# Optimization experiments

Measured on AMD Instinct MI355X. Metric: run time of the kernel, lower is better.

The kernel has to match this reference:

```python
import jax, jax.numpy as jnp
import numpy as np

B, L, K, S, D, H, C = 32, 256, 50, 16, 128, 4, 128
V, NN, NU, NS = 50000, 100000, 50000, 5000


def mha(q, k, v, in_w, in_b, out_w, out_b, n_heads):
    # PyTorch nn.MultiheadAttention (batch_first, eval mode) semantics.
    d = q.shape[-1]
    hd = d // n_heads
    wq, wk, wv = jnp.split(in_w, 3, axis=0)
    bq, bk, bv = jnp.split(in_b, 3)
    def heads(t):
        return t.reshape(t.shape[:-1] + (n_heads, hd))
    qh = heads(q @ wq.T + bq)
    kh = heads(k @ wk.T + bk)
    vh = heads(v @ wv.T + bv)
    scores = jnp.einsum('...qhd,...khd->...hqk', qh, kh) / jnp.sqrt(jnp.asarray(hd, q.dtype))
    attn = jax.nn.softmax(scores, axis=-1)
    o = jnp.einsum('...hqk,...khd->...qhd', attn, vh)
    o = o.reshape(o.shape[:-2] + (d,))
    return o @ out_w.T + out_b


def conv1d(x, w, b):
    # x: [B, D, L], w: [Cout, D, k]
    y = jax.lax.conv_general_dilated(x, w, (1,), 'VALID', dimension_numbers=('NCH', 'OIH', 'NCH'))
    return y + b[None, :, None]


def meta_path_module(paths, gru_wih, gru_whh, gru_bih, gru_bhh, in_w, in_b, out_w, out_b, ln_g, ln_b):
    # paths: [B, S, T, D] -> [B, D]
    b, s, t, d = paths.shape
    x = paths.reshape(b * s, t, d)
    def step(h, xt):
        gi = xt @ gru_wih.T + gru_bih
        gh = h @ gru_whh.T + gru_bhh
        ir, iz, inn = jnp.split(gi, 3, axis=-1)
        hr, hz, hn = jnp.split(gh, 3, axis=-1)
        r = jax.nn.sigmoid(ir + hr)
        z = jax.nn.sigmoid(iz + hz)
        n = jnp.tanh(inn + r * hn)
        return (1.0 - z) * n + z * h, None
    h0 = jnp.zeros((b * s, d), paths.dtype)
    h, _ = jax.lax.scan(step, h0, jnp.swapaxes(x, 0, 1))
    enc = h.reshape(b, s, d)
    attn = mha(enc, enc, enc, in_w, in_b, out_w, out_b, H)
    y = enc + attn
    mu = jnp.mean(y, -1, keepdims=True)
    var = jnp.var(y, -1, keepdims=True)
    y = (y - mu) / jnp.sqrt(var + 1e-5) * ln_g + ln_b
    return jnp.mean(y, axis=1)


def _forward(word_table, news_table, user_table, source_table,
             wa_in_w, wa_in_b, wa_out_w, wa_out_b,
             conv_w3, conv_b3, conv_w4, conv_b4, conv_w5, conv_b5, fc_w, fc_b,
             nsn_gru_wih, nsn_gru_whh, nsn_gru_bih, nsn_gru_bhh,
             nsn_in_w, nsn_in_b, nsn_out_w, nsn_out_b, nsn_ln_g, nsn_ln_b,
             nun_gru_wih, nun_gru_whh, nun_gru_bih, nun_gru_bhh,
             nun_in_w, nun_in_b, nun_out_w, nun_out_b, nun_ln_g, nun_ln_b,
             mp_w1, mp_b1, mp_w2, mp_b2, cls_w1, cls_b1, cls_w2, cls_b2,
             news_ids, news_word_indices, word_ctx_ids, nsn_src, nsn_end, nun_usr, nun_end):
    # --- fine-grained word embeds: per-token query attending over context news ---
    base = word_table[news_word_indices]              # [B, L, D]
    ctx = news_table[word_ctx_ids]                    # [B, L, K, D] (dominant gather)
    q = base[:, :, None, :]                           # [B, L, 1, D]
    fine = mha(q, ctx, ctx, wa_in_w, wa_in_b, wa_out_w, wa_out_b, H)[:, :, 0, :]
    pad = (news_word_indices == 0)[..., None]
    doc = jnp.where(pad, jnp.zeros((), base.dtype), fine)   # padding_idx=0 -> zeros
    # --- coarse CNN encoder ---
    x = jnp.swapaxes(doc, 1, 2)                       # [B, D, L]
    pooled = [jnp.max(jax.nn.relu(conv1d(x, w, b)), axis=2)
              for w, b in ((conv_w3, conv_b3), (conv_w4, conv_b4), (conv_w5, conv_b5))]
    semantic = jnp.concatenate(pooled, axis=1) @ fc_w.T + fc_b   # [B, D]
    # --- meta-path interaction ---
    start = jnp.broadcast_to(news_table[news_ids][:, None, :], (B, S, D))
    nsn_paths = jnp.stack([start, source_table[nsn_src], news_table[nsn_end]], axis=2)
    nun_paths = jnp.stack([start, user_table[nun_usr], news_table[nun_end]], axis=2)
    nsn_e = meta_path_module(nsn_paths, nsn_gru_wih, nsn_gru_whh, nsn_gru_bih, nsn_gru_bhh,
                             nsn_in_w, nsn_in_b, nsn_out_w, nsn_out_b, nsn_ln_g, nsn_ln_b)
    nun_e = meta_path_module(nun_paths, nun_gru_wih, nun_gru_whh, nun_gru_bih, nun_gru_bhh,
                             nun_in_w, nun_in_b, nun_out_w, nun_out_b, nun_ln_g, nun_ln_b)
    stack = jnp.stack([nsn_e, nun_e], axis=1)         # [B, 2, D]
    sc = jnp.tanh(stack @ mp_w1.T + mp_b1) @ mp_w2.T + mp_b2
    w = jax.nn.softmax(sc, axis=1)
    struct = jnp.sum(stack * w, axis=1)
    comb = jnp.concatenate([semantic, struct], axis=1)
    hcls = jax.nn.relu(comb @ cls_w1.T + cls_b1)
    return hcls @ cls_w2.T + cls_b2                   # [B, 2]


def setup_inputs() -> dict:
    key = jax.random.key(0)
    ks = iter(jax.random.split(key, 80))
    def p(shape):
        return (jax.random.normal(next(ks), shape, jnp.float32) * 0.02)
    inp = {}
    inp['news_ids'] = jax.random.randint(next(ks), (B,), 0, NN)
    inp['news_word_indices'] = jax.random.randint(next(ks), (B, L), 0, V)
    inp['word_ctx_ids'] = jax.random.randint(next(ks), (B, L, K), 0, NN)
    inp['nsn_src'] = jax.random.randint(next(ks), (B, S), 0, NS)
    inp['nsn_end'] = jax.random.randint(next(ks), (B, S), 0, NN)
    inp['nun_usr'] = jax.random.randint(next(ks), (B, S), 0, NU)
    inp['nun_end'] = jax.random.randint(next(ks), (B, S), 0, NN)
    inp['word_table'] = p((V, D)).at[0].set(0.0)
    inp['news_table'] = p((NN, D))
    inp['user_table'] = p((NU, D))
    inp['source_table'] = p((NS, D))
    inp['wa_in_w'] = p((3 * D, D)); inp['wa_in_b'] = p((3 * D,))
    inp['wa_out_w'] = p((D, D)); inp['wa_out_b'] = p((D,))
    for k in (3, 4, 5):
        inp[f'conv_w{k}'] = p((C, D, k)); inp[f'conv_b{k}'] = p((C,))
    inp['fc_w'] = p((D, 3 * C)); inp['fc_b'] = p((D,))
    for pre in ('nsn', 'nun'):
        inp[f'{pre}_gru_wih'] = p((3 * D, D)); inp[f'{pre}_gru_whh'] = p((3 * D, D))
        inp[f'{pre}_gru_bih'] = p((3 * D,)); inp[f'{pre}_gru_bhh'] = p((3 * D,))
        inp[f'{pre}_in_w'] = p((3 * D, D)); inp[f'{pre}_in_b'] = p((3 * D,))
        inp[f'{pre}_out_w'] = p((D, D)); inp[f'{pre}_out_b'] = p((D,))
        inp[f'{pre}_ln_g'] = jnp.ones((D,), jnp.float32); inp[f'{pre}_ln_b'] = jnp.zeros((D,), jnp.float32)
    inp['mp_w1'] = p((D // 2, D)); inp['mp_b1'] = p((D // 2,))
    inp['mp_w2'] = p((1, D // 2)); inp['mp_b2'] = p((1,))
    inp['cls_w1'] = p((D, 2 * D)); inp['cls_b1'] = p((D,))
    inp['cls_w2'] = p((2, D)); inp['cls_b2'] = p((2,))
    return inp


def reference(word_table, news_table, user_table, source_table,
              wa_in_w, wa_in_b, wa_out_w, wa_out_b,
              conv_w3, conv_b3, conv_w4, conv_b4, conv_w5, conv_b5, fc_w, fc_b,
              nsn_gru_wih, nsn_gru_whh, nsn_gru_bih, nsn_gru_bhh,
              nsn_in_w, nsn_in_b, nsn_out_w, nsn_out_b, nsn_ln_g, nsn_ln_b,
              nun_gru_wih, nun_gru_whh, nun_gru_bih, nun_gru_bhh,
              nun_in_w, nun_in_b, nun_out_w, nun_out_b, nun_ln_g, nun_ln_b,
              mp_w1, mp_b1, mp_w2, mp_b2, cls_w1, cls_b1, cls_w2, cls_b2,
              news_ids, news_word_indices, word_ctx_ids, nsn_src, nsn_end, nun_usr, nun_end):
    return _forward(word_table, news_table, user_table, source_table,
                    wa_in_w, wa_in_b, wa_out_w, wa_out_b,
                    conv_w3, conv_b3, conv_w4, conv_b4, conv_w5, conv_b5, fc_w, fc_b,
                    nsn_gru_wih, nsn_gru_whh, nsn_gru_bih, nsn_gru_bhh,
                    nsn_in_w, nsn_in_b, nsn_out_w, nsn_out_b, nsn_ln_g, nsn_ln_b,
                    nun_gru_wih, nun_gru_whh, nun_gru_bih, nun_gru_bhh,
                    nun_in_w, nun_in_b, nun_out_w, nun_out_b, nun_ln_g, nun_ln_b,
                    mp_w1, mp_b1, mp_w2, mp_b2, cls_w1, cls_b1, cls_w2, cls_b2,
                    news_ids, news_word_indices, word_ctx_ids, nsn_src, nsn_end, nun_usr, nun_end)
```

## Files before the change

### kernel.cpp

```cpp
#include <hip/hip_runtime.h>
#include <hip/hip_bf16.h>

#define BB 32
#define LL 256
#define KC 50
#define SS 16
#define DD 128
#define NH 4
#define CC 128
#define VV 50000
#define NNN 100000
#define NUU 50000
#define NSS 5000

typedef __attribute__((ext_vector_type(8))) short bf16x8;
typedef __attribute__((ext_vector_type(8))) unsigned short u16x8;
typedef __attribute__((ext_vector_type(4))) float f32x4;

#define APAD 132

__device__ __forceinline__ float dot4(float4 a, float4 b){
  return a.x*b.x + a.y*b.y + a.z*b.z + a.w*b.w;
}

__device__ __forceinline__ unsigned short f2bf(float f){
  union { float f; unsigned int u; } v; v.f = f;
  unsigned int r = (v.u + 0x7FFFu + ((v.u >> 16) & 1u)) >> 16;
  return (unsigned short)r;
}
__device__ __forceinline__ float bf2f(unsigned short s){
  union { unsigned int u; float f; } v; v.u = ((unsigned int)s) << 16;
  return v.f;
}

__global__ __launch_bounds__(256) void k_prep(
    const float* __restrict__ w3, const float* __restrict__ w4,
    const float* __restrict__ w5,
    const float* __restrict__ wih0, const float* __restrict__ whh0,
    const float* __restrict__ wih1, const float* __restrict__ whh1,
    const float* __restrict__ in_w, const float* __restrict__ out_w,
    const float* __restrict__ inw0, const float* __restrict__ outw0,
    const float* __restrict__ inw1, const float* __restrict__ outw1,
    unsigned short* __restrict__ wb3, unsigned short* __restrict__ wb4,
    unsigned short* __restrict__ wb5, unsigned short* __restrict__ wgb,
    unsigned short* __restrict__ wab, unsigned short* __restrict__ wmh){
  int e = blockIdx.x*256 + threadIdx.x;
  if (e < CC*DD*3){ int c=e/(DD*3), rm=e%(DD*3), d=rm/3, jj=rm%3;
    wb3[((size_t)jj*CC + c)*DD + d] = f2bf(w3[e]); }
  if (e < CC*DD*4){ int c=e/(DD*4), rm=e%(DD*4), d=rm/4, jj=rm%4;
    wb4[((size_t)jj*CC + c)*DD + d] = f2bf(w4[e]); }
  if (e < CC*DD*5){ int c=e/(DD*5), rm=e%(DD*5), d=rm/5, jj=rm%5;
    wb5[((size_t)jj*CC + c)*DD + d] = f2bf(w5[e]); }
  if (e < 384*DD){
    wgb[e]          = f2bf(wih0[e]);
    wgb[49152 + e]  = f2bf(whh0[e]);
    wgb[98304 + e]  = f2bf(wih1[e]);
    wgb[147456 + e] = f2bf(whh1[e]);
    wab[e]          = f2bf(in_w[e]);
  }
  if (e >= 384*DD && e < 512*DD) wab[e] = f2bf(out_w[e - 384*DD]);
  if (e < 512*DD){
    float s0 = (e < 384*DD) ? inw0[e] : outw0[e - 384*DD];
    float s1 = (e < 384*DD) ? inw1[e] : outw1[e - 384*DD];
    wmh[e]                 = f2bf(s0);
    wmh[(size_t)512*DD + e] = f2bf(s1);
  }
}

__global__ __launch_bounds__(256) void k_projkv(
    const float* __restrict__ news, const unsigned short* __restrict__ wkvb,
    const float* __restrict__ in_b, unsigned short* __restrict__ nK,
    unsigned short* __restrict__ nV){
  const int tid  = threadIdx.x;
  const int wave = tid >> 6;
  const int lane = tid & 63;
  const int l15  = lane & 15;
  const int quad = lane >> 4;
  const int r0   = blockIdx.x * 16;
  const int nw0  = wave * 64;

  const float* src = news + (size_t)(r0 + l15)*DD + quad*8;
  bf16x8 afr[4];
  #pragma unroll
  for (int ks=0; ks<4; ks++){
    float4 v0 = *(const float4*)(src + ks*32);
    float4 v1 = *(const float4*)(src + ks*32 + 4);
    bf16x8 a;
    a[0]=(short)f2bf(v0.x); a[1]=(short)f2bf(v0.y); a[2]=(short)f2bf(v0.z); a[3]=(short)f2bf(v0.w);
    a[4]=(short)f2bf(v1.x); a[5]=(short)f2bf(v1.y); a[6]=(short)f2bf(v1.z); a[7]=(short)f2bf(v1.w);
    afr[ks] = a;
  }
  unsigned short* outp = (nw0 < 128) ? nK : nV;
  const int cbase = nw0 & 127;
  #pragma unroll
  for (int nt=0; nt<4; nt++){
    const int n0 = nw0 + nt*16;
    bf16x8 bfr[4];
    #pragma unroll
    for (int ks=0; ks<4; ks++)
      bfr[ks] = *(const bf16x8*)(wkvb + (size_t)(n0 + l15)*DD + ks*32 + quad*8);
    const float bias = in_b[128 + n0 + l15];
    f32x4 acc = {0.f,0.f,0.f,0.f};
    #pragma unroll
    for (int ks=0; ks<4; ks++)
      acc = __builtin_amdgcn_mfma_f32_16x16x32_bf16(afr[ks], bfr[ks], acc, 0,0,0);
    const int c = cbase + nt*16 + l15;
    #pragma unroll
    for (int r=0;r<4;r++)
      outp[(size_t)(r0 + quad*4 + r)*DD + c] = f2bf(acc[r] + bias);
  }
}

__global__ __launch_bounds__(64) void k_qh(
    const float* __restrict__ word_table, const int* __restrict__ widx,
    const unsigned short* __restrict__ wqb, const float* __restrict__ in_b,
    float* __restrict__ qh){
  const int lane = threadIdx.x;
  const int l15 = lane & 15, quad = lane >> 4;
  const int p0 = blockIdx.x * 16;
  const int row = widx[p0 + l15];
  const float* src = word_table + (size_t)row*DD + quad*8;
  bf16x8 afr[4];
  #pragma unroll
  for (int ks=0; ks<4; ks++){
    float4 v0 = *(const float4*)(src + ks*32);
    float4 v1 = *(const float4*)(src + ks*32 + 4);
    bf16x8 a;
    a[0]=(short)f2bf(v0.x); a[1]=(short)f2bf(v0.y); a[2]=(short)f2bf(v0.z); a[3]=(short)f2bf(v0.w);
    a[4]=(short)f2bf(v1.x); a[5]=(short)f2bf(v1.y); a[6]=(short)f2bf(v1.z); a[7]=(short)f2bf(v1.w);
    afr[ks] = a;
  }
  #pragma unroll
  for (int nt=0; nt<8; nt++){
    const int n0 = nt*16;
    bf16x8 bfr[4];
    #pragma unroll
    for (int ks=0; ks<4; ks++)
      bfr[ks] = *(const bf16x8*)(wqb + (size_t)(n0+l15)*DD + ks*32 + quad*8);
    const float bias = in_b[n0 + l15];
    f32x4 acc = {0.f,0.f,0.f,0.f};
    #pragma unroll
    for (int ks=0; ks<4; ks++)
      acc = __builtin_amdgcn_mfma_f32_16x16x32_bf16(afr[ks], bfr[ks], acc, 0,0,0);
    #pragma unroll
    for (int r=0;r<4;r++){
      int m = quad*4 + r;
      qh[(size_t)(p0+m)*DD + n0 + l15] = acc[r] + bias;
    }
  }
}

__global__ __launch_bounds__(64) void k_attn(
    const float* __restrict__ qh, const unsigned short* __restrict__ nK,
    const unsigned short* __restrict__ nV, const int* __restrict__ ctx_ids,
    unsigned short* __restrict__ o_out){
  const int p = blockIdx.x;
  const int lane = threadIdx.x;
  const int r = lane >> 4;
  const int g = lane & 15;
  const int h = g >> 2;
  __shared__ int ids[52];
  __shared__ float sc[NH][52];
  if (lane < KC) ids[lane] = ctx_ids[(size_t)p*KC + lane];
  float qv[8];
  {
    const float4* qp = (const float4*)(qh + (size_t)p*DD + g*8);
    float4 q0 = qp[0], q1 = qp[1];
    qv[0]=q0.x; qv[1]=q0.y; qv[2]=q0.z; qv[3]=q0.w;
    qv[4]=q1.x; qv[5]=q1.y; qv[6]=q1.z; qv[7]=q1.w;
  }
  __syncthreads();
  for (int kb=0; kb<13; kb++){
    int k2 = kb*4 + r;
    int row = ids[(k2 < KC) ? k2 : 0];
    u16x8 kv = *(const u16x8*)(nK + (size_t)row*DD + g*8);
    float pr = 0.f;
    #pragma unroll
    for (int j=0;j<8;j++) pr += qv[j]*bf2f(kv[j]);
    pr += __shfl_xor(pr, 1, 64);
    pr += __shfl_xor(pr, 2, 64);
    if ((g & 3) == 0 && k2 < KC) sc[h][k2] = pr;
  }
  __syncthreads();
  {
    const int hh = lane >> 4, kc = lane & 15;
    const float scale = 0.17677669529663687f;
    float mx = -1e30f;
    #pragma unroll
    for (int q4=0;q4<4;q4++){ int k2=kc+q4*16; if (k2<KC) mx = fmaxf(mx, sc[hh][k2]); }
    mx = fmaxf(mx, __shfl_xor(mx, 1, 64));
    mx = fmaxf(mx, __shfl_xor(mx, 2, 64));
    mx = fmaxf(mx, __shfl_xor(mx, 4, 64));
    mx = fmaxf(mx, __shfl_xor(mx, 8, 64));
    float sm = 0.f;
    float ev[4];
    #pragma unroll
    for (int q4=0;q4<4;q4++){
      int k2=kc+q4*16;
      ev[q4] = (k2<KC) ? __expf((sc[hh][k2]-mx)*scale) : 0.f;
      sm += ev[q4];
    }
    sm += __shfl_xor(sm, 1, 64);
    sm += __shfl_xor(sm, 2, 64);
    sm += __shfl_xor(sm, 4, 64);
    sm += __shfl_xor(sm, 8, 64);
    float inv = 1.f/sm;
    #pragma unroll
    for (int q4=0;q4<4;q4++){ int k2=kc+q4*16; if (k2<KC) sc[hh][k2] = ev[q4]*inv; }
  }
  __syncthreads();
  float acc[8];
  #pragma unroll
  for (int j=0;j<8;j++) acc[j]=0.f;
  for (int kb=0; kb<13; kb++){
    int k2 = kb*4 + r;
    int row = ids[(k2 < KC) ? k2 : 0];
    float w = (k2 < KC) ? sc[h][k2] : 0.f;
    u16x8 vv = *(const u16x8*)(nV + (size_t)row*DD + g*8);
    #pragma unroll
    for (int j=0;j<8;j++) acc[j] += w*bf2f(vv[j]);
  }
  #pragma unroll
  for (int j=0;j<8;j++){
    acc[j] += __shfl_xor(acc[j], 16, 64);
    acc[j] += __shfl_xor(acc[j], 32, 64);
  }
  if (r == 0){
    u16x8 o;
    #pragma unroll
    for (int j=0;j<8;j++) o[j] = f2bf(acc[j]);
    *(u16x8*)(o_out + (size_t)p*DD + g*8) = o;
  }
}

__global__ __launch_bounds__(64) void k_wo(
    const unsigned short* __restrict__ o_attn, const int* __restrict__ widx,
    const unsigned short* __restrict__ wob, const float* __restrict__ out_b,
    unsigned short* __restrict__ doc){
  const int lane = threadIdx.x;
  const int l15 = lane & 15, quad = lane >> 4;
  const int p0 = blockIdx.x * 16;
  bf16x8 afr[4];
  #pragma unroll
  for (int ks=0; ks<4; ks++)
    afr[ks] = *(const bf16x8*)(o_attn + (size_t)(p0+l15)*DD + ks*32 + quad*8);
  int msk[4];
  #pragma unroll
  for (int r=0;r<4;r++) msk[r] = widx[p0 + quad*4 + r];
  #pragma unroll
  for (int nt=0; nt<8; nt++){
    const int n0 = nt*16;
    bf16x8 bfr[4];
    #pragma unroll
    for (int ks=0; ks<4; ks++)
      bfr[ks] = *(const bf16x8*)(wob + (size_t)(n0+l15)*DD + ks*32 + quad*8);
    const float bias = out_b[n0 + l15];
    f32x4 acc = {0.f,0.f,0.f,0.f};
    #pragma unroll
    for (int ks=0; ks<4; ks++)
      acc = __builtin_amdgcn_mfma_f32_16x16x32_bf16(afr[ks], bfr[ks], acc, 0,0,0);
    #pragma unroll
    for (int r=0;r<4;r++){
      int m = quad*4 + r;
      doc[(size_t)(p0+m)*DD + n0 + l15] = (msk[r] == 0) ? (unsigned short)0
                                                        : f2bf(acc[r] + bias);
    }
  }
}

#define CROWS 68
#define CPAD 136
__global__ __launch_bounds__(256) void k_conv(
    const unsigned short* __restrict__ doc, const unsigned short* __restrict__ wb3,
    const unsigned short* __restrict__ wb4, const unsigned short* __restrict__ wb5,
    float* __restrict__ convp){
  __shared__ __align__(16) char smem[CROWS*CPAD*2];
  unsigned short* ds = (unsigned short*)smem;
  float* smf = (float*)smem;
  const int blk = blockIdx.x;
  const int chunk = blk & 3;
  const int j = (blk >> 2) % 3;
  const int b = blk / 12;
  const int kk = 3 + j;
  const int T = LL - kk + 1;
  const int t0 = chunk * 64;
  const int nrows = 64 + kk - 1;
  const unsigned short* wb = (j==0) ? wb3 : (j==1) ? wb4 : wb5;
  const int tid = threadIdx.x;
  for (int i = tid; i < nrows*16; i += 256){
    int row = i >> 4, q8 = i & 15;
    int gt = t0 + row;
    u16x8 v = (u16x8){0,0,0,0,0,0,0,0};
    if (gt < LL) v = *(const u16x8*)(doc + ((size_t)b*LL + gt)*DD + q8*8);
    *(u16x8*)(ds + row*CPAD + q8*8) = v;
  }
  __syncthreads();
  const int wave = tid >> 6;
  const int lane = tid & 63;
  const int l15  = lane & 15;
  const int quad = lane >> 4;
  f32x4 acc[8];
  #pragma unroll
  for (int nt=0;nt<8;nt++) acc[nt] = (f32x4){0.f,0.f,0.f,0.f};
  for (int jj=0; jj<kk; jj++){
    #pragma unroll
    for (int ks=0; ks<4; ks++){
      bf16x8 af = *(const bf16x8*)(ds + (wave*16 + l15 + jj)*CPAD + ks*32 + quad*8);
      #pragma unroll
      for (int nt=0; nt<8; nt++){
        bf16x8 bf = *(const bf16x8*)(wb + ((size_t)jj*CC + nt*16 + l15)*DD + ks*32 + quad*8);
        acc[nt] = __builtin_amdgcn_mfma_f32_16x16x32_bf16(af, bf, acc[nt], 0,0,0);
      }
    }
  }
  __syncthreads();
  #pragma unroll
  for (int nt=0; nt<8; nt++){
    float mx = -1e30f;
    #pragma unroll
    for (int r=0;r<4;r++){
      int t = t0 + wave*16 + quad*4 + r;
      mx = fmaxf(mx, (t < T) ? acc[nt][r] : -1e30f);
    }
    mx = fmaxf(mx, __shfl_xor(mx, 16, 64));
    mx = fmaxf(mx, __shfl_xor(mx, 32, 64));
    if (quad == 0) smf[wave*128 + nt*16 + l15] = mx;
  }
  __syncthreads();
  if (tid < 128){
    float m4 = fmaxf(fmaxf(smf[tid], smf[128+tid]), fmaxf(smf[256+tid], smf[384+tid]));
    convp[(((size_t)b*3 + j)*4 + chunk)*CC + tid] = m4;
  }
}

#define GSTR 392
__global__ __launch_bounds__(256) void k_gru(
    const float* __restrict__ news_table, const float* __restrict__ user_table,
    const float* __restrict__ source_table,
    const int* __restrict__ news_ids, const int* __restrict__ nsn_src,
    const int* __restrict__ nsn_end, const int* __restrict__ nun_usr,
    const int* __restrict__ nun_end,
    const unsigned short* __restrict__ wgb,
    const float* __restrict__ bih0, const float* __restrict__ bhh0,
    const float* __restrict__ bih1, const float* __restrict__ bhh1,
    float* __restrict__ enc){
  __shared__ __align__(16) unsigned short xs[16][CPAD];
  __shared__ __align__(16) unsigned short hs[16][CPAD];
  __shared__ float hf[8][128];
  __shared__ float gi[8][GSTR];
  __shared__ float gh[8][GSTR];
  const int blk = blockIdx.x;
  const int m  = blk >> 6;
  const int b  = (blk >> 1) & 31;
  const int s0 = (blk & 1) * 8;
  const int tid = threadIdx.x;
  const int wave = tid >> 6, lane = tid & 63, l15 = lane & 15, quad = lane >> 4;
  const unsigned short* Wih = wgb + (size_t)m*2*384*DD;
  const unsigned short* Whh = Wih + 384*DD;
  const float* bih = m ? bih1 : bih0;
  const float* bhh = m ? bhh1 : bhh0;
  for (int i=tid;i<16*CPAD;i+=256){ (&xs[0][0])[i]=0; (&hs[0][0])[i]=0; }
  for (int i=tid;i<8*128;i+=256) (&hf[0][0])[i]=0.f;
  __syncthreads();
  for (int t=0;t<3;t++){
    {
      int s = tid >> 5, j = tid & 31;
      int row; const float* tab;
      if (t==0){ row = news_ids[b]; tab = news_table; }
      else if (t==1){ row = m ? nun_usr[b*SS+s0+s] : nsn_src[b*SS+s0+s];
                      tab = m ? user_table : source_table; }
      else { row = m ? nun_end[b*SS+s0+s] : nsn_end[b*SS+s0+s]; tab = news_table; }
      float4 v = ((const float4*)(tab + (size_t)row*DD))[j];
      unsigned short* dp = &xs[s][j*4];
      dp[0]=f2bf(v.x); dp[1]=f2bf(v.y); dp[2]=f2bf(v.z); dp[3]=f2bf(v.w);
    }
    __syncthreads();
    bf16x8 ax[4], ah[4];
    #pragma unroll
    for (int ks=0;ks<4;ks++){
      ax[ks] = *(const bf16x8*)&xs[l15][ks*32+quad*8];
      ah[ks] = *(const bf16x8*)&hs[l15][ks*32+quad*8];
    }
    #pragma unroll
    for (int nt=0;nt<6;nt++){
      const int n0 = wave*96 + nt*16;
      f32x4 ga = {0.f,0.f,0.f,0.f}, ha = {0.f,0.f,0.f,0.f};
      #pragma unroll
      for (int ks=0;ks<4;ks++){
        bf16x8 bi = *(const bf16x8*)(Wih + (size_t)(n0+l15)*DD + ks*32+quad*8);
        ga = __builtin_amdgcn_mfma_f32_16x16x32_bf16(ax[ks], bi, ga, 0,0,0);
        bf16x8 bh = *(const bf16x8*)(Whh + (size_t)(n0+l15)*DD + ks*32+quad*8);
        ha = __builtin_amdgcn_mfma_f32_16x16x32_bf16(ah[ks], bh, ha, 0,0,0);
      }
      if (quad < 2){
        #pragma unroll
        for (int r=0;r<4;r++){
          gi[quad*4+r][n0+l15] = ga[r];
          gh[quad*4+r][n0+l15] = ha[r];
        }
      }
    }
    __syncthreads();
    #pragma unroll
    for (int k=0;k<4;k++){
      int it = tid + k*256;
      int s = it >> 7, g = it & 127;
      float rr = 1.f/(1.f+__expf(-(gi[s][g] + gh[s][g] + bih[g] + bhh[g])));
      float zz = 1.f/(1.f+__expf(-(gi[s][128+g] + gh[s][128+g] + bih[128+g] + bhh[128+g])));
      float nn = tanhf(gi[s][256+g] + bih[256+g] + rr*(gh[s][256+g] + bhh[256+g]));
      float hnew = (1.f-zz)*nn + zz*hf[s][g];
      hf[s][g] = hnew;
      hs[s][g] = f2bf(hnew);
    }
    __syncthreads();
  }
  {
    int s = tid >> 5, j = tid & 31;
    float4 v = ((const float4*)hf[s])[j];
    ((float4*)(enc + (((size_t)m*BB + b)*SS + (s0+s))*DD))[j] = v;
  }
}

#define MPAD 136
__global__ __launch_bounds__(256) void k_metamha(
    const float* __restrict__ enc,
    const unsigned short* __restrict__ wmh,
    const float* __restrict__ inb0, const float* __restrict__ outb0,
    const float* __restrict__ lng0, const float* __restrict__ lnb0,
    const float* __restrict__ inb1, const float* __restrict__ outb1,
    const float* __restrict__ lng1, const float* __restrict__ lnb1,
    float* __restrict__ meta_e){
  const int m = blockIdx.x >> 5;
  const int b = blockIdx.x & 31;
  const int tid = threadIdx.x;
  const int wave = tid >> 6, lane = tid & 63, l15 = lane & 15, quad = lane >> 4;
  const unsigned short* W = wmh + (size_t)m*512*DD;
  const float* in_b  = m ? inb1 : inb0;
  const float* out_b = m ? outb1 : outb0;
  const float* lng   = m ? lng1 : lng0;
  const float* lnb   = m ? lnb1 : lnb0;

  __shared__ __align__(16) unsigned short ebf[16][MPAD];
  __shared__ __align__(16) unsigned short qb[16][MPAD];
  __shared__ __align__(16) unsigned short kb[16][MPAD];
  __shared__ __align__(16) unsigned short ob[16][MPAD];
  __shared__ float vf[16][128];
  __shared__ float er[16][132];
  __shared__ float at[NH][16][16];
  __shared__ float mu[16], rs[16];
  __shared__ float part[2][128];

  const float* esrc = enc + ((size_t)m*BB + b)*SS*DD;
  for (int i = tid; i < 16*32; i += 256){
    int s = i >> 5, j = i & 31;
    float4 v = ((const float4*)esrc)[i];
    ((float4*)er[s])[j] = v;
    unsigned short* dp = &ebf[s][j*4];
    dp[0]=f2bf(v.x); dp[1]=f2bf(v.y); dp[2]=f2bf(v.z); dp[3]=f2bf(v.w);
  }
  __syncthreads();
  {
    bf16x8 ax[4];
    #pragma unroll
    for (int ks=0;ks<4;ks++) ax[ks] = *(const bf16x8*)&ebf[l15][ks*32+quad*8];
    #pragma unroll
    for (int nt=0; nt<6; nt++){
      const int n0 = wave*96 + nt*16;
      f32x4 acc = {0.f,0.f,0.f,0.f};
      #pragma unroll
      for (int ks=0;ks<4;ks++){
        bf16x8 bw = *(const bf16x8*)(W + (size_t)(n0+l15)*DD + ks*32+quad*8);
        acc = __builtin_amdgcn_mfma_f32_16x16x32_bf16(ax[ks], bw, acc, 0,0,0);
      }
      const float bias = in_b[n0+l15];
      const int col = n0 + l15;
      #pragma unroll
      for (int r=0;r<4;r++){
        int row = quad*4+r;
        float val = acc[r] + bias;
        if (n0 < 128)      qb[row][col]       = f2bf(val);
        else if (n0 < 256) kb[row][col-128]   = f2bf(val);
        else               vf[row][col-256]   = val;
      }
    }
  }
  __syncthreads();
  {
    const int h = wave;
    bf16x8 aq = *(const bf16x8*)&qb[l15][h*32 + quad*8];
    bf16x8 ak = *(const bf16x8*)&kb[l15][h*32 + quad*8];
    f32x4 z = {0.f,0.f,0.f,0.f};
    f32x4 acc = __builtin_amdgcn_mfma_f32_16x16x32_bf16(aq, ak, z, 0,0,0);
    #pragma unroll
    for (int r=0;r<4;r++)
      at[h][quad*4+r][l15] = acc[r] * 0.17677669529663687f;
  }
  __syncthreads();
  if (tid < 64){
    int h = tid>>4, qi = tid&15;
    float mx=-1e30f;
    #pragma unroll
    for (int ki=0;ki<16;ki++) mx = fmaxf(mx, at[h][qi][ki]);
    float sm=0.f;
    float ee[16];
    #pragma unroll
    for (int ki=0;ki<16;ki++){ ee[ki]=__expf(at[h][qi][ki]-mx); sm+=ee[ki]; }
    float inv=1.f/sm;
    #pragma unroll
    for (int ki=0;ki<16;ki++) at[h][qi][ki]=ee[ki]*inv;
  }
  __syncthreads();
  {
    int c = tid & 127, h = c >> 5;
    int sBase = (tid >> 7) * 8;
    #pragma unroll
    for (int s=0;s<8;s++){
      float acc=0.f;
      #pragma unroll
      for (int ki=0;ki<16;ki++) acc += at[h][sBase+s][ki]*vf[ki][c];
      ob[sBase+s][c] = f2bf(acc);
    }
  }
  __syncthreads();
  {
    bf16x8 ao[4];
    #pragma unroll
    for (int ks=0;ks<4;ks++) ao[ks] = *(const bf16x8*)&ob[l15][ks*32+quad*8];
    #pragma unroll
    for (int nt=0; nt<2; nt++){
      const int n0 = wave*32 + nt*16;
      f32x4 acc = {0.f,0.f,0.f,0.f};
      #pragma unroll
      for (int ks=0;ks<4;ks++){
        bf16x8 bw = *(const bf16x8*)(W + (size_t)(384 + n0+l15)*DD + ks*32+quad*8);
        acc = __builtin_amdgcn_mfma_f32_16x16x32_bf16(ao[ks], bw, acc, 0,0,0);
      }
      const float bias = out_b[n0+l15];
      const int col = n0 + l15;
      #pragma unroll
      for (int r=0;r<4;r++){
        int row = quad*4 + r;
        er[row][col] += acc[r] + bias;
      }
    }
  }
  __syncthreads();
  {
    int row = tid >> 4, i = tid & 15;
    const float* yr = &er[row][i*8];
    float s1=0.f, s2=0.f;
    #pragma unroll
    for (int j2=0;j2<8;j2++){ float y=yr[j2]; s1+=y; s2+=y*y; }
    #pragma unroll
    for (int msk=1; msk<16; msk<<=1){
      s1 += __shfl_xor(s1, msk, 64);
      s2 += __shfl_xor(s2, msk, 64);
    }
    if (i==0){
      float mean = s1*(1.f/128.f);
      mu[row]=mean;
      rs[row]=rsqrtf(s2*(1.f/128.f) - mean*mean + 1e-5f);
    }
  }
  __syncthreads();
  {
    int c = tid & 127, half = tid >> 7;
    float g = lng[c], bb2 = lnb[c];
    float acc=0.f;
    #pragma unroll
    for (int s=0;s<8;s++){
      int ss = half*8+s;
      acc += (er[ss][c]-mu[ss])*rs[ss]*g + bb2;
    }
    part[half][c]=acc;
  }
  __syncthreads();
  if (tid < 128)
    meta_e[((size_t)m*BB+b)*DD + tid] = (part[0][tid]+part[1][tid]) * (1.f/16.f);
}

__global__ __launch_bounds__(128) void k_final(
    const float* __restrict__ convp,
    const float* __restrict__ cb3, const float* __restrict__ cb4,
    const float* __restrict__ cb5,
    const float* __restrict__ fc_w, const float* __restrict__ fc_b,
    const float* __restrict__ meta_e,
    const float* __restrict__ mp_w1, const float* __restrict__ mp_b1,
    const float* __restrict__ mp_w2, const float* __restrict__ mp_b2,
    const float* __restrict__ cls_w1, const float* __restrict__ cls_b1,
    const float* __restrict__ cls_w2, const float* __restrict__ cls_b2,
    float* __restrict__ out){
  const int b = blockIdx.x;
  const int c = threadIdx.x;
  __shared__ float pooled[384];
  __shared__ float comb[256];
  __shared__ float hcls[128];
  __shared__ float tt[2][64];
  __shared__ float wsc[2];
  for (int idx=c; idx<384; idx+=128){
    int j = idx >> 7, cc2 = idx & 127;
    const float* base = convp + (((size_t)b*3 + j)*4)*CC + cc2;
    float mx = -1e30f;
    for (int ci=0;ci<4;ci++) mx = fmaxf(mx, base[ci*CC]);
    const float* cb = (j==0)?cb3:(j==1)?cb4:cb5;
    pooled[idx] = fmaxf(mx + cb[cc2], 0.f);
  }
  __syncthreads();
  {
    float acc = fc_b[c];
    const float* wr = fc_w + (size_t)c*384;
    for (int i=0;i<384;i++) acc += pooled[i]*wr[i];
    comb[c] = acc;
  }
  if (c < 64){
    for (int m=0;m<2;m++){
      const float* ev = meta_e + ((size_t)m*BB+b)*DD;
      float acc = mp_b1[c];
      const float* wr = mp_w1 + (size_t)c*DD;
      for (int i=0;i<DD;i++) acc += ev[i]*wr[i];
      tt[m][c] = tanhf(acc);
    }
  }
  __syncthreads();
  if (c == 0){
    float s0 = mp_b2[0], s1 = mp_b2[0];
    for (int j=0;j<64;j++){ s0 += tt[0][j]*mp_w2[j]; s1 += tt[1][j]*mp_w2[j]; }
    float mx = fmaxf(s0,s1);
    float e0 = __expf(s0-mx), e1 = __expf(s1-mx);
    wsc[0] = e0/(e0+e1); wsc[1] = e1/(e0+e1);
  }
  __syncthreads();
  comb[128+c] = wsc[0]*meta_e[((size_t)b)*DD + c]
              + wsc[1]*meta_e[((size_t)(BB+b))*DD + c];
  __syncthreads();
  {
    float acc = cls_b1[c];
    const float* wr = cls_w1 + (size_t)c*256;
    for (int i=0;i<256;i++) acc += comb[i]*wr[i];
    hcls[c] = fmaxf(acc, 0.f);
  }
  __syncthreads();
  if (c < 2){
    float acc = cls_b2[c];
    const float* wr = cls_w2 + (size_t)c*DD;
    for (int i=0;i<DD;i++) acc += hcls[i]*wr[i];
    out[b*2 + c] = acc;
  }
}

extern "C" void kernel_launch(void* const* d_in, const int* in_sizes, int n_in,
                              void* d_out, int out_size, void* d_ws, size_t ws_size,
                              hipStream_t stream){
  const int* news_ids = (const int*)d_in[0];
  const int* nwi      = (const int*)d_in[1];
  const int* ctx_ids  = (const int*)d_in[2];
  const int* nsn_src  = (const int*)d_in[3];
  const int* nsn_end  = (const int*)d_in[4];
  const int* nun_usr  = (const int*)d_in[5];
  const int* nun_end  = (const int*)d_in[6];
  const float* word_table   = (const float*)d_in[7];
  const float* news_table   = (const float*)d_in[8];
  const float* user_table   = (const float*)d_in[9];
  const float* source_table = (const float*)d_in[10];
  const float* wa_in_w  = (const float*)d_in[11];
  const float* wa_in_b  = (const float*)d_in[12];
  const float* wa_out_w = (const float*)d_in[13];
  const float* wa_out_b = (const float*)d_in[14];
  const float* conv_w3 = (const float*)d_in[15];
  const float* conv_b3 = (const float*)d_in[16];
  const float* conv_w4 = (const float*)d_in[17];
  const float* conv_b4 = (const float*)d_in[18];
  const float* conv_w5 = (const float*)d_in[19];
  const float* conv_b5 = (const float*)d_in[20];
  const float* fc_w = (const float*)d_in[21];
  const float* fc_b = (const float*)d_in[22];
  const float* wih0 = (const float*)d_in[23];
  const float* whh0 = (const float*)d_in[24];
  const float* bih0 = (const float*)d_in[25];
  const float* bhh0 = (const float*)d_in[26];
  const float* inw0 = (const float*)d_in[27];
  const float* inb0 = (const float*)d_in[28];
  const float* outw0 = (const float*)d_in[29];
  const float* outb0 = (const float*)d_in[30];
  const float* lng0 = (const float*)d_in[31];
  const float* lnb0 = (const float*)d_in[32];
  const float* wih1 = (const float*)d_in[33];
  const float* whh1 = (const float*)d_in[34];
  const float* bih1 = (const float*)d_in[35];
  const float* bhh1 = (const float*)d_in[36];
  const float* inw1 = (const float*)d_in[37];
  const float* inb1 = (const float*)d_in[38];
  const float* outw1 = (const float*)d_in[39];
  const float* outb1 = (const float*)d_in[40];
  const float* lng1 = (const float*)d_in[41];
  const float* lnb1 = (const float*)d_in[42];
  const float* mp_w1 = (const float*)d_in[43];
  const float* mp_b1 = (const float*)d_in[44];
  const float* mp_w2 = (const float*)d_in[45];
  const float* mp_b2 = (const float*)d_in[46];
  const float* cls_w1 = (const float*)d_in[47];
  const float* cls_b1 = (const float*)d_in[48];
  const float* cls_w2 = (const float*)d_in[49];
  const float* cls_b2 = (const float*)d_in[50];

  char* wsb = (char*)d_ws;
  unsigned short* nK = (unsigned short*)wsb;
  unsigned short* nV = nK + (size_t)NNN*DD;
  unsigned short* wb3 = nV + (size_t)NNN*DD;
  unsigned short* wb4 = wb3 + (size_t)CC*DD*3;
  unsigned short* wb5 = wb4 + (size_t)CC*DD*4;
  unsigned short* wgb = wb5 + (size_t)CC*DD*5;
  unsigned short* wab = wgb + (size_t)4*384*DD;
  unsigned short* wmh = wab + (size_t)512*DD;
  float* qh     = (float*)(wmh + (size_t)2*512*DD);
  unsigned short* o_at = (unsigned short*)(qh + (size_t)BB*LL*DD);
  unsigned short* doc  = (unsigned short*)((float*)o_at + (size_t)BB*LL*DD);
  float* convp  = (float*)doc + (size_t)BB*LL*DD;
  float* enc    = convp + BB*3*4*CC;
  float* meta_e = enc + (size_t)2*BB*SS*DD;
  const size_t need_bytes = (size_t)((char*)(meta_e + 2*BB*DD) - wsb);
  if (ws_size < need_bytes) return;

  const unsigned short* wqb  = wab;
  const unsigned short* wkvb = wab + (size_t)128*DD;
  const unsigned short* wob  = wab + (size_t)384*DD;

  k_prep<<<dim3(320), dim3(256), 0, stream>>>(conv_w3, conv_w4, conv_w5,
      wih0, whh0, wih1, whh1, wa_in_w, wa_out_w,
      inw0, outw0, inw1, outw1,
      wb3, wb4, wb5, wgb, wab, wmh);
  k_projkv<<<dim3(NNN/16), dim3(256), 0, stream>>>(news_table, wkvb, wa_in_b, nK, nV);
  k_qh<<<dim3(BB*LL/16), dim3(64), 0, stream>>>(word_table, nwi, wqb, wa_in_b, qh);
  k_attn<<<dim3(BB*LL), dim3(64), 0, stream>>>(qh, nK, nV, ctx_ids, o_at);
  k_wo<<<dim3(BB*LL/16), dim3(64), 0, stream>>>(o_at, nwi, wob, wa_out_b, doc);
  k_conv<<<dim3(BB*3*4), dim3(256), 0, stream>>>(doc, wb3, wb4, wb5, convp);
  k_gru<<<dim3(128), dim3(256), 0, stream>>>(news_table, user_table, source_table,
      news_ids, nsn_src, nsn_end, nun_usr, nun_end,
      wgb, bih0, bhh0, bih1, bhh1, enc);
  k_metamha<<<dim3(64), dim3(256), 0, stream>>>(enc, wmh,
      inb0, outb0, lng0, lnb0,
      inb1, outb1, lng1, lnb1, meta_e);
  k_final<<<dim3(BB), dim3(128), 0, stream>>>(convp, conv_b3, conv_b4, conv_b5,
      fc_w, fc_b, meta_e, mp_w1, mp_b1, mp_w2, mp_b2,
      cls_w1, cls_b1, cls_w2, cls_b2, (float*)d_out);
}
```

Baseline: 404.7 us.

## Restructure K/V projection to one wave per tile with LDS-staged coalesced stores

The K/V projection kernel now runs one wave per 16-row tile instead of four waves that each reload the same activation rows. The MFMA operands are swapped so each lane holds four consecutive output columns, which allows vectorized bias loads and packed 8-byte writes into shared memory. Output rows are then written to global memory as coalesced 8-byte stores instead of scattered 2-byte stores. In exchange, each wave does four times more MFMA work serially, and the kernel gains a shared-memory round trip and a barrier.

```diff
diff --git a/kernel.cpp b/kernel.cpp
--- a/kernel.cpp
+++ b/kernel.cpp
@@ -67,18 +67,15 @@
   }
 }
 
-__global__ __launch_bounds__(256) void k_projkv(
+#define PKSTR 272
+__global__ __launch_bounds__(64) void k_projkv(
     const float* __restrict__ news, const unsigned short* __restrict__ wkvb,
     const float* __restrict__ in_b, unsigned short* __restrict__ nK,
     unsigned short* __restrict__ nV){
-  const int tid  = threadIdx.x;
-  const int wave = tid >> 6;
-  const int lane = tid & 63;
-  const int l15  = lane & 15;
-  const int quad = lane >> 4;
-  const int r0   = blockIdx.x * 16;
-  const int nw0  = wave * 64;
-
+  __shared__ __align__(16) unsigned short os[16*PKSTR];
+  const int lane = threadIdx.x;
+  const int l15 = lane & 15, quad = lane >> 4;
+  const int r0 = blockIdx.x * 16;
   const float* src = news + (size_t)(r0 + l15)*DD + quad*8;
   bf16x8 afr[4];
   #pragma unroll
@@ -90,24 +87,32 @@
     a[4]=(short)f2bf(v1.x); a[5]=(short)f2bf(v1.y); a[6]=(short)f2bf(v1.z); a[7]=(short)f2bf(v1.w);
     afr[ks] = a;
   }
-  unsigned short* outp = (nw0 < 128) ? nK : nV;
-  const int cbase = nw0 & 127;
-  #pragma unroll
-  for (int nt=0; nt<4; nt++){
-    const int n0 = nw0 + nt*16;
-    bf16x8 bfr[4];
+  #pragma unroll
+  for (int nt=0; nt<16; nt++){
+    const int n0 = nt*16;
+    bf16x8 wfr[4];
     #pragma unroll
     for (int ks=0; ks<4; ks++)
-      bfr[ks] = *(const bf16x8*)(wkvb + (size_t)(n0 + l15)*DD + ks*32 + quad*8);
-    const float bias = in_b[128 + n0 + l15];
+      wfr[ks] = *(const bf16x8*)(wkvb + (size_t)(n0 + l15)*DD + ks*32 + quad*8);
     f32x4 acc = {0.f,0.f,0.f,0.f};
     #pragma unroll
     for (int ks=0; ks<4; ks++)
-      acc = __builtin_amdgcn_mfma_f32_16x16x32_bf16(afr[ks], bfr[ks], acc, 0,0,0);
-    const int c = cbase + nt*16 + l15;
-    #pragma unroll
-    for (int r=0;r<4;r++)
-      outp[(size_t)(r0 + quad*4 + r)*DD + c] = f2bf(acc[r] + bias);
+      acc = __builtin_amdgcn_mfma_f32_16x16x32_bf16(wfr[ks], afr[ks], acc, 0,0,0);
+    float4 bias = *(const float4*)(in_b + 128 + n0 + quad*4);
+    unsigned short pk[4];
+    pk[0] = f2bf(acc[0] + bias.x);
+    pk[1] = f2bf(acc[1] + bias.y);
+    pk[2] = f2bf(acc[2] + bias.z);
+    pk[3] = f2bf(acc[3] + bias.w);
+    *(unsigned long long*)(os + l15*PKSTR + n0 + quad*4) = *(const unsigned long long*)pk;
+  }
+  __syncthreads();
+  unsigned short* outp = (lane < 32) ? nK : nV;
+  const int col = (lane*4) & 127;
+  #pragma unroll
+  for (int j=0; j<16; j++){
+    unsigned long long v = *(const unsigned long long*)(os + j*PKSTR + lane*4);
+    *(unsigned long long*)(outp + (size_t)(r0 + j)*DD + col) = v;
   }
 }
 
@@ -729,7 +734,7 @@
       wih0, whh0, wih1, whh1, wa_in_w, wa_out_w,
       inw0, outw0, inw1, outw1,
       wb3, wb4, wb5, wgb, wab, wmh);
-  k_projkv<<<dim3(NNN/16), dim3(256), 0, stream>>>(news_table, wkvb, wa_in_b, nK, nV);
+  k_projkv<<<dim3(NNN/16), dim3(64), 0, stream>>>(news_table, wkvb, wa_in_b, nK, nV);
   k_qh<<<dim3(BB*LL/16), dim3(64), 0, stream>>>(word_table, nwi, wqb, wa_in_b, qh);
   k_attn<<<dim3(BB*LL), dim3(64), 0, stream>>>(qh, nK, nV, ctx_ids, o_at);
   k_wo<<<dim3(BB*LL/16), dim3(64), 0, stream>>>(o_at, nwi, wob, wa_out_b, doc);
```

Result: faster. 390.4 us (-3.5%).

## Tile K/V projection over 80 rows per block with register-resident weights and staged stores

Applied to the files above, without the earlier changes.

The K/V projection kernel now processes 80 news rows per block instead of 16. Each wave keeps its 64x128 weight slice in registers for five row tiles, and the fp32 inputs are converted to bf16 once into shared memory. The MFMA operands are swapped so results come out transposed, then staged through LDS so each lane writes 8-byte contiguous chunks to global memory. This amortizes weight loads and improves store coalescing, at the cost of more registers and LDS per block and fewer blocks in the grid.

```diff
diff --git a/kernel.cpp b/kernel.cpp
--- a/kernel.cpp
+++ b/kernel.cpp
@@ -67,47 +67,76 @@
   }
 }
 
+#define PST 136
+#define TST 72
 __global__ __launch_bounds__(256) void k_projkv(
     const float* __restrict__ news, const unsigned short* __restrict__ wkvb,
     const float* __restrict__ in_b, unsigned short* __restrict__ nK,
     unsigned short* __restrict__ nV){
+  __shared__ __align__(16) unsigned short As[80*PST];
+  __shared__ __align__(16) unsigned short Tw[4*16*TST];
   const int tid  = threadIdx.x;
   const int wave = tid >> 6;
   const int lane = tid & 63;
   const int l15  = lane & 15;
   const int quad = lane >> 4;
-  const int r0   = blockIdx.x * 16;
-  const int nw0  = wave * 64;
-
-  const float* src = news + (size_t)(r0 + l15)*DD + quad*8;
-  bf16x8 afr[4];
-  #pragma unroll
-  for (int ks=0; ks<4; ks++){
-    float4 v0 = *(const float4*)(src + ks*32);
-    float4 v1 = *(const float4*)(src + ks*32 + 4);
-    bf16x8 a;
-    a[0]=(short)f2bf(v0.x); a[1]=(short)f2bf(v0.y); a[2]=(short)f2bf(v0.z); a[3]=(short)f2bf(v0.w);
-    a[4]=(short)f2bf(v1.x); a[5]=(short)f2bf(v1.y); a[6]=(short)f2bf(v1.z); a[7]=(short)f2bf(v1.w);
-    afr[ks] = a;
-  }
-  unsigned short* outp = (nw0 < 128) ? nK : nV;
-  const int cbase = nw0 & 127;
-  #pragma unroll
-  for (int nt=0; nt<4; nt++){
-    const int n0 = nw0 + nt*16;
-    bf16x8 bfr[4];
+  const int r0   = blockIdx.x * 80;
+  const int cw   = wave * 64;
+
+  bf16x8 wfr[4][4];
+  #pragma unroll
+  for (int nt=0; nt<4; nt++)
     #pragma unroll
     for (int ks=0; ks<4; ks++)
-      bfr[ks] = *(const bf16x8*)(wkvb + (size_t)(n0 + l15)*DD + ks*32 + quad*8);
-    const float bias = in_b[128 + n0 + l15];
-    f32x4 acc = {0.f,0.f,0.f,0.f};
+      wfr[nt][ks] = *(const bf16x8*)(wkvb + (size_t)(cw + nt*16 + l15)*DD + ks*32 + quad*8);
+  float4 bv[4];
+  #pragma unroll
+  for (int nt=0; nt<4; nt++)
+    bv[nt] = *(const float4*)(in_b + 128 + cw + nt*16 + quad*4);
+
+  for (int i = tid; i < 80*32; i += 256){
+    int row = i >> 5, j = i & 31;
+    float4 v = ((const float4*)(news + (size_t)(r0 + row)*DD))[j];
+    unsigned short* d = As + row*PST + j*4;
+    d[0]=f2bf(v.x); d[1]=f2bf(v.y); d[2]=f2bf(v.z); d[3]=f2bf(v.w);
+  }
+  __syncthreads();
+
+  unsigned short* outp = (wave < 2) ? nK : nV;
+  const int cwo = (wave & 1) * 64;
+  unsigned short* tw = Tw + wave*16*TST;
+  const int rr = lane >> 4;
+  const int cc = lane & 15;
+
+  #pragma unroll
+  for (int mt=0; mt<5; mt++){
+    bf16x8 afr[4];
     #pragma unroll
     for (int ks=0; ks<4; ks++)
-      acc = __builtin_amdgcn_mfma_f32_16x16x32_bf16(afr[ks], bfr[ks], acc, 0,0,0);
-    const int c = cbase + nt*16 + l15;
-    #pragma unroll
-    for (int r=0;r<4;r++)
-      outp[(size_t)(r0 + quad*4 + r)*DD + c] = f2bf(acc[r] + bias);
+      afr[ks] = *(const bf16x8*)(As + (mt*16 + l15)*PST + ks*32 + quad*8);
+    f32x4 acc[4];
+    #pragma unroll
+    for (int nt=0; nt<4; nt++) acc[nt] = (f32x4){0.f,0.f,0.f,0.f};
+    #pragma unroll
+    for (int ks=0; ks<4; ks++)
+      #pragma unroll
+      for (int nt=0; nt<4; nt++)
+        acc[nt] = __builtin_amdgcn_mfma_f32_16x16x32_bf16(wfr[nt][ks], afr[ks], acc[nt], 0,0,0);
+    #pragma unroll
+    for (int nt=0; nt<4; nt++){
+      unsigned short pk[4];
+      pk[0] = f2bf(acc[nt][0] + bv[nt].x);
+      pk[1] = f2bf(acc[nt][1] + bv[nt].y);
+      pk[2] = f2bf(acc[nt][2] + bv[nt].z);
+      pk[3] = f2bf(acc[nt][3] + bv[nt].w);
+      *(unsigned long long*)(tw + l15*TST + nt*16 + quad*4) = *(const unsigned long long*)pk;
+    }
+    const int gr0 = r0 + mt*16;
+    #pragma unroll
+    for (int s=0; s<4; s++){
+      unsigned long long v = *(const unsigned long long*)(tw + (s*4 + rr)*TST + cc*4);
+      *(unsigned long long*)(outp + (size_t)(gr0 + s*4 + rr)*DD + cwo + cc*4) = v;
+    }
   }
 }
 
@@ -729,7 +758,7 @@
       wih0, whh0, wih1, whh1, wa_in_w, wa_out_w,
       inw0, outw0, inw1, outw1,
       wb3, wb4, wb5, wgb, wab, wmh);
-  k_projkv<<<dim3(NNN/16), dim3(256), 0, stream>>>(news_table, wkvb, wa_in_b, nK, nV);
+  k_projkv<<<dim3(NNN/80), dim3(256), 0, stream>>>(news_table, wkvb, wa_in_b, nK, nV);
   k_qh<<<dim3(BB*LL/16), dim3(64), 0, stream>>>(word_table, nwi, wqb, wa_in_b, qh);
   k_attn<<<dim3(BB*LL), dim3(64), 0, stream>>>(qh, nK, nV, ctx_ids, o_at);
   k_wo<<<dim3(BB*LL/16), dim3(64), 0, stream>>>(o_at, nwi, wob, wa_out_b, doc);
```

New measurement: 359.0 us. 1.13x faster.
